# Kernel optimization log

Hardware: AMD Instinct MI355X
Metric: run time of the kernel (lower is better)

The kernel has to match this reference:

```python
import jax, jax.numpy as jnp
import numpy as np

C, P, H, W, BS = 256, 2, 128, 128, 4
NH, DH = 16, 16
NPATCH = (H // P) * (W // P)   # 4096
NTOK = NPATCH + 1              # 4097 with cls token
NMASK = int((1 - 0.75) * NTOK) # 1024 kept (visible) tokens
PRED = 512
NUM_BLOCKS = 1

def _sincos_pos_embed(embed_dim, h, w):
    # faithful port of get_2d_sincos_pos_embed
    def emb1d(d, pos):
        omega = np.arange(d // 2, dtype=np.float64) / (d / 2.0)
        omega = 1.0 / 10000 ** omega
        out = np.einsum('m,d->md', pos.reshape(-1), omega)
        return np.concatenate([np.sin(out), np.cos(out)], axis=1)
    gh = np.arange(h, dtype=np.float32)
    gw = np.arange(w, dtype=np.float32)
    grid = np.stack(np.meshgrid(gw, gh), axis=0).reshape(2, 1, h, w)
    emb = np.concatenate([emb1d(embed_dim // 2, grid[0]), emb1d(embed_dim // 2, grid[1])], axis=1)
    return jnp.asarray(emb, jnp.float32)  # [h*w, embed_dim]

def _ln(x, g, b, eps=1e-5):
    mu = x.mean(-1, keepdims=True)
    var = ((x - mu) ** 2).mean(-1, keepdims=True)
    return (x - mu) * jax.lax.rsqrt(var + eps) * g + b

def _gelu(x):
    return jax.nn.gelu(x, approximate=False)  # torch nn.GELU default (erf)

def _attn(x, qkv_w, qkv_b, proj_w, proj_b, nq_g, nq_b, nk_g, nk_b):
    bs, n, c = x.shape
    qkv = x @ qkv_w + qkv_b
    q, k, v = jnp.split(qkv, 3, axis=-1)
    heads = lambda t: t.reshape(bs, n, NH, DH).transpose(0, 2, 1, 3)  # [b,h,n,d]
    q, k, v = heads(q), heads(k), heads(v)
    q = _ln(q, nq_g, nq_b)  # per-head-dim QK LayerNorm
    k = _ln(k, nk_g, nk_b)
    score = jnp.einsum('bhnd,bhmd->bhnm', q, k) / np.float32(np.sqrt(DH))
    attn = jax.nn.softmax(score, axis=-1)
    attn_map = attn.mean(axis=1)[:, 0, 1:]  # [b, n-1]
    out = jnp.einsum('bhnm,bhmd->bhnd', attn, v)
    out = out.transpose(0, 2, 1, 3).reshape(bs, n, c)
    return out @ proj_w + proj_b, attn_map

def _forward(mask_index, x, Wp, bp, cls, qkv_w, qkv_b, proj_w, proj_b, nq_g, nq_b, nk_g, nk_b,
             conv_w, conv_b, ca1_w, ca1_b, ca2_w, ca2_b, mlp1_w, mlp1_b, mlp2_w, mlp2_b,
             node_w, ln0_g, ln0_b, h1_w, h1_b, ln1_g, ln1_b, h2_w, h2_b, ln2_g, ln2_b,
             h3_w, h3_b, pr_w, pr_b):
    bs = x.shape[0]
    # PatchEmbed: conv stride=kernel=P expressed as reshape + einsum
    xp = x.reshape(bs, 3, H // P, P, W // P, P)
    tok = jnp.einsum('bchpwq,ocpq->bohw', xp, Wp) + bp[None, :, None, None]
    tok = tok.reshape(bs, C, NPATCH).transpose(0, 2, 1)  # [b, l, c]
    tok = tok + _sincos_pos_embed(C, H // P, W // P)[None]
    tok = jnp.concatenate([jnp.broadcast_to(cls, (bs, 1, C)), tok], axis=1)  # prepend cls
    # mask_img: keep NMASK tokens per the precomputed permutation prefix
    m = jnp.take_along_axis(tok, mask_index[:, :, None], axis=1)  # [b, NMASK, C]

    attn_map = None
    for blk in range(NUM_BLOCKS):
        feat = m[..., None]  # feature_list: [b, l, c, width]
        for i in range(4):
            j = blk * 4 + i
            xl = feat[..., -1]
            o1 = _gelu(xl @ conv_w[j] + conv_b[j])  # Conv1x1Act
            gate = jax.nn.sigmoid(jax.nn.relu(xl @ ca1_w[j] + ca1_b[j]) @ ca2_w[j] + ca2_b[j])
            o2 = gate * xl                           # ChannelAttention
            o4 = _gelu(xl @ mlp1_w[j] + mlp1_b[j]) @ mlp2_w[j] + mlp2_b[j]  # MLP
            cat = jnp.concatenate([feat, jnp.stack([o1, o2, xl, o4], axis=-1)], axis=-1)  # width 5+i
            wmix = jax.nn.softmax(node_w[j, :5 + i] / 0.01)
            mixed = jnp.einsum('blcn,n->blc', cat, wmix)
            a_out, attn_map = _attn(mixed, qkv_w[j], qkv_b[j], proj_w[j], proj_b[j],
                                    nq_g[j], nq_b[j], nk_g[j], nk_b[j])
            xo = a_out + mixed  # residual
            feat = jnp.concatenate([feat, xo[..., None]], axis=-1)
        m = xo
    # Predict_head (tokenwise)
    h = _ln(m, ln0_g, ln0_b)
    h = h @ h1_w + h1_b
    h = _ln(h, ln1_g, ln1_b)
    h = h @ h2_w + h2_b
    h = _ln(h, ln2_g, ln2_b)
    h = h @ h3_w + h3_b
    return h @ pr_w + pr_b  # [b, NMASK, PRED]

def setup_inputs():
    key = jax.random.key(0)
    ks = iter(jax.random.split(key, 64))
    rn = lambda shape, s=0.02: jax.random.normal(next(ks), shape, jnp.float32) * s
    noise = jax.random.normal(next(ks), (BS, NTOK))
    mask_index = jnp.argsort(noise, axis=-1)[:, :NMASK].astype(jnp.int32)
    return dict(
        x=jax.random.normal(next(ks), (BS, 3, H, W), jnp.float32),
        mask_index=mask_index,
        Wp=rn((C, 3, P, P)), bp=jnp.zeros((C,)), cls=rn((1, 1, C)),
        qkv_w=rn((4, C, 3 * C)), qkv_b=jnp.zeros((4, 3 * C)),
        proj_w=rn((4, C, C)), proj_b=jnp.zeros((4, C)),
        nq_g=jnp.ones((4, DH)), nq_b=jnp.zeros((4, DH)),
        nk_g=jnp.ones((4, DH)), nk_b=jnp.zeros((4, DH)),
        conv_w=rn((4, C, C)), conv_b=jnp.zeros((4, C)),
        ca1_w=rn((4, C, C // 16)), ca1_b=jnp.zeros((4, C // 16)),
        ca2_w=rn((4, C // 16, C)), ca2_b=jnp.zeros((4, C)),
        mlp1_w=rn((4, C, 4 * C)), mlp1_b=jnp.zeros((4, 4 * C)),
        mlp2_w=rn((4, 4 * C, C)), mlp2_b=jnp.zeros((4, C)),
        node_w=jax.random.normal(next(ks), (4, 8), jnp.float32),
        ln0_g=jnp.ones((C,)), ln0_b=jnp.zeros((C,)),
        h1_w=rn((C, 2048)), h1_b=jnp.zeros((2048,)),
        ln1_g=jnp.ones((2048,)), ln1_b=jnp.zeros((2048,)),
        h2_w=rn((2048, 256)), h2_b=jnp.zeros((256,)),
        ln2_g=jnp.ones((256,)), ln2_b=jnp.zeros((256,)),
        h3_w=rn((256, 2048)), h3_b=jnp.zeros((2048,)),
        pr_w=rn((2048, PRED)), pr_b=jnp.zeros((PRED,)),
    )

def reference(x, mask_index, Wp, bp, cls, qkv_w, qkv_b, proj_w, proj_b, nq_g, nq_b, nk_g, nk_b,
              conv_w, conv_b, ca1_w, ca1_b, ca2_w, ca2_b, mlp1_w, mlp1_b, mlp2_w, mlp2_b,
              node_w, ln0_g, ln0_b, h1_w, h1_b, ln1_g, ln1_b, h2_w, h2_b, ln2_g, ln2_b,
              h3_w, h3_b, pr_w, pr_b):
    return _forward(mask_index, x, Wp, bp, cls, qkv_w, qkv_b, proj_w, proj_b, nq_g, nq_b, nk_g, nk_b,
                    conv_w, conv_b, ca1_w, ca1_b, ca2_w, ca2_b, mlp1_w, mlp1_b, mlp2_w, mlp2_b,
                    node_w, ln0_g, ln0_b, h1_w, h1_b, ln1_g, ln1_b, h2_w, h2_b, ln2_g, ln2_b,
                    h3_w, h3_b, pr_w, pr_b)
```

## Files before the change

kernel.cpp:

```cpp
#include <hip/hip_runtime.h>
#include <math.h>
#include <cstddef>

#define RTOK 4096
#define CDIM 256
#define NHEAD 16
#define DHEAD 16
#define SEQ 1024
#define BSZ 4

#define ACT_NONE 0
#define ACT_GELU 1

typedef short short8 __attribute__((ext_vector_type(8)));
typedef float f32x4  __attribute__((ext_vector_type(4)));
typedef _Float16 half8 __attribute__((ext_vector_type(8)));
typedef _Float16 half4 __attribute__((ext_vector_type(4)));

__device__ __forceinline__ float gelu_erf(float x) {
    return 0.5f * x * (1.0f + erff(x * 0.70710678118654752f));
}
__device__ __forceinline__ unsigned short f2b(float f) {
    unsigned u = __float_as_uint(f);
    unsigned r = (u + 0x7FFFu + ((u >> 16) & 1u)) >> 16;
    return (unsigned short)r;
}
__device__ __forceinline__ float b2f(unsigned short u) {
    return __uint_as_float((unsigned)u << 16);
}
__device__ __forceinline__ void gld16(const unsigned short* g, unsigned short* l) {
    __builtin_amdgcn_global_load_lds(
        (const __attribute__((address_space(1))) unsigned int*)g,
        (__attribute__((address_space(3))) unsigned int*)l, 16, 0, 0);
}
__device__ __forceinline__ float node_wsel(const float* nwp, int cnt, int widx) {
    float ww[8];
    float mx = -1e30f;
    for (int t = 0; t < cnt; ++t) { ww[t] = nwp[t] * 100.0f; mx = fmaxf(mx, ww[t]); }
    float ssum = 0.0f;
    for (int t = 0; t < cnt; ++t) { ww[t] = expf(ww[t] - mx); ssum += ww[t]; }
    return ww[widx] / ssum;
}

struct WtSeg { const float* in; unsigned short* out; int K, N, ntx, tpz, zin, zout; };
struct WtTab { WtSeg s[9]; int cum[10]; };

__global__ __launch_bounds__(256) void wtrans_all(WtTab tab)
{
    int g = blockIdx.x;
    int si = 0;
    #pragma unroll
    for (int i = 0; i < 8; ++i) if (g >= tab.cum[i + 1]) si = i + 1;
    WtSeg sg = tab.s[si];
    int t = g - tab.cum[si];
    int z = t / sg.tpz, r = t % sg.tpz;
    int kb = (r % sg.ntx) * 32, nb = (r / sg.ntx) * 32;
    const float* in = sg.in + (size_t)z * sg.zin;
    unsigned short* out = sg.out + (size_t)z * sg.zout;

    __shared__ float tt[32][33];
    int tx = threadIdx.x & 31, ty = threadIdx.x >> 5;
    #pragma unroll
    for (int rr = 0; rr < 4; ++rr) {
        int kk = ty * 4 + rr;
        tt[kk][tx] = in[(size_t)(kb + kk) * sg.N + nb + tx];
    }
    __syncthreads();
    #pragma unroll
    for (int rr = 0; rr < 4; ++rr) {
        int nn = ty * 4 + rr;
        out[(size_t)(nb + nn) * sg.K + kb + tx] = f2b(tt[tx][nn]);
    }
}

__global__ __launch_bounds__(256) void embed_kernel(
    const float* __restrict__ x, const int* __restrict__ mask_index,
    const float* __restrict__ Wp, const float* __restrict__ bp,
    const float* __restrict__ cls,
    float* __restrict__ out, unsigned short* __restrict__ outb)
{
    int row = blockIdx.x;
    int b = row >> 10;
    int c = threadIdx.x;
    int idx = mask_index[row];
    if (idx == 0) {
        float v = cls[c];
        out[(size_t)row * 256 + c] = v;
        outb[(size_t)row * 256 + c] = f2b(v);
        return;
    }
    int p  = idx - 1;
    int ph = p >> 6, pw = p & 63;

    __shared__ float xs[12];
    if (c < 12) {
        int ch = c >> 2, r = (c >> 1) & 1, q = c & 1;
        xs[c] = x[(((size_t)b * 3 + ch) * 128 + (ph * 2 + r)) * 128 + (pw * 2 + q)];
    }
    __syncthreads();

    float acc = bp[c];
    #pragma unroll
    for (int t = 0; t < 12; ++t) acc += xs[t] * Wp[c * 12 + t];

    int part = c >> 6, cc = c & 63;
    double omega = exp((double)cc * -0.14391156831212787);
    double posv  = (part < 2) ? (double)pw : (double)ph;
    double a     = posv * omega;
    double e     = ((part & 1) == 0) ? sin(a) : cos(a);
    float v = acc + (float)e;
    out[(size_t)row * 256 + c] = v;
    outb[(size_t)row * 256 + c] = f2b(v);
}

template<int MT, int ACT, bool RES, bool FOUT, int BMODE, bool SPLIT, int NW>
__global__ __launch_bounds__(256) void gemm_mfma(
    const unsigned short* __restrict__ A, const unsigned short* __restrict__ Bt,
    const float* __restrict__ bias, const float* __restrict__ bias1,
    const float* __restrict__ Rsd,
    float* __restrict__ C, unsigned short* __restrict__ Cb,
    int M, int N, int K, int N0,
    const float* __restrict__ nwp, int ncnt, int widx)
{
    constexpr int BM = 64 * MT;
    __shared__ __align__(16) unsigned short As[BM * 64];
    __shared__ __align__(16) unsigned short Bs[64 * 64];
    int tid = threadIdx.x;
    int w = tid >> 6, lane = tid & 63;
    int l15 = lane & 15, q = lane >> 4;

    int gx = gridDim.x, gy = gridDim.y;
    int L = blockIdx.x + gx * blockIdx.y;
    int xcd = L & 7, j = L >> 3;
    int by = xcd * (gy >> 3) + j / gx;
    int bx = j - (j / gx) * gx;
    int row0 = by * BM, col0 = bx * 64;

    f32x4 acc[MT][4];
    #pragma unroll
    for (int mt = 0; mt < MT; ++mt)
        #pragma unroll
        for (int nt = 0; nt < 4; ++nt)
            acc[mt][nt] = (f32x4){0.f, 0.f, 0.f, 0.f};

    for (int kb = 0; kb < K; kb += 64) {
        __syncthreads();
        #pragma unroll
        for (int t = 0; t < 2 * MT; ++t) {
            int slot = tid + t * 256;
            int r = slot >> 3;
            int s = (slot & 7) ^ (r & 7);
            gld16(A + (size_t)(row0 + r) * K + kb + s * 8, &As[slot * 8]);
        }
        #pragma unroll
        for (int t = 0; t < 2; ++t) {
            int slot = tid + t * 256;
            int r = slot >> 3;
            int s = (slot & 7) ^ (r & 7);
            gld16(Bt + (size_t)(col0 + r) * K + kb + s * 8, &Bs[slot * 8]);
        }
        __syncthreads();

        #pragma unroll
        for (int hh = 0; hh < 2; ++hh) {
            short8 af[MT];
            #pragma unroll
            for (int mt = 0; mt < MT; ++mt) {
                int R = w * 16 * MT + mt * 16 + l15;
                int c = hh * 4 + q;
                af[mt] = *(const short8*)&As[R * 64 + ((c ^ (R & 7)) << 3)];
            }
            #pragma unroll
            for (int nt = 0; nt < 4; ++nt) {
                int R = nt * 16 + l15;
                int c = hh * 4 + q;
                short8 bf = *(const short8*)&Bs[R * 64 + ((c ^ (R & 7)) << 3)];
                #pragma unroll
                for (int mt = 0; mt < MT; ++mt)
                    acc[mt][nt] = __builtin_amdgcn_mfma_f32_16x16x32_bf16(
                        af[mt], bf, acc[mt][nt], 0, 0, 0);
            }
        }
    }

    float wsel = 0.0f;
    if (NW > 0) wsel = node_wsel(nwp, ncnt, widx);

    #pragma unroll
    for (int mt = 0; mt < MT; ++mt) {
        #pragma unroll
        for (int nt = 0; nt < 4; ++nt) {
            #pragma unroll
            for (int reg = 0; reg < 4; ++reg) {
                int row = row0 + w * 16 * MT + mt * 16 + q * 4 + reg;
                int col = col0 + nt * 16 + l15;
                if (SPLIT) {
                    float v = acc[mt][nt][reg] +
                              (col < N0 ? bias[col] : bias1[col - N0]);
                    if (ACT == ACT_GELU) v = gelu_erf(v);
                    if (col < N0) {
                        if (NW == 1) C[(size_t)row * N0 + col] += wsel * v;
                        else         C[(size_t)row * N0 + col] = v;
                    } else {
                        Cb[(size_t)row * (N - N0) + (col - N0)] = f2b(v);
                    }
                } else {
                    float v = acc[mt][nt][reg] + bias[col];
                    if (ACT == ACT_GELU) v = gelu_erf(v);
                    if (NW == 2) v = wsel * v + Rsd[(size_t)row * N + col];
                    else if (RES) v += Rsd[(size_t)row * N + col];
                    if (FOUT) C[(size_t)row * N + col] = v;
                    if (BMODE == 1) Cb[(size_t)row * N + col] = f2b(v);
                    if (BMODE == 2) {
                        _Float16 hv = (_Float16)v;
                        Cb[(size_t)row * N + col] = *(unsigned short*)&hv;
                    }
                }
            }
        }
    }
}

__global__ __launch_bounds__(256) void chanattn_kernel(
    const float* __restrict__ xl,
    const float* f0, const float* f1, const float* f2,
    const float* __restrict__ ca1w, const float* __restrict__ ca1b,
    const float* __restrict__ ca2w, const float* __restrict__ ca2b,
    const float* __restrict__ node_w, int cnt,
    float* __restrict__ MIX)
{
    __shared__ float xs[256];
    __shared__ float sm16[16];
    size_t row = blockIdx.x;
    int tid = threadIdx.x;
    xs[tid] = xl[row * 256 + tid];
    __syncthreads();

    int h = tid >> 4, part = tid & 15;
    float p = 0.f;
    #pragma unroll
    for (int i = 0; i < 16; ++i)
        p += xs[part * 16 + i] * ca1w[(part * 16 + i) * 16 + h];
    p += __shfl_down(p, 8, 16);
    p += __shfl_down(p, 4, 16);
    p += __shfl_down(p, 2, 16);
    p += __shfl_down(p, 1, 16);
    if (part == 0) sm16[h] = fmaxf(p + ca1b[h], 0.0f);
    __syncthreads();

    float g = ca2b[tid];
    #pragma unroll
    for (int hh = 0; hh < 16; ++hh) g += sm16[hh] * ca2w[hh * 256 + tid];
    g = 1.0f / (1.0f + expf(-g));
    float o2 = g * xs[tid];

    float ww[8];
    float mx = -1e30f;
    for (int t = 0; t < cnt; ++t) { ww[t] = node_w[t] * 100.0f; mx = fmaxf(mx, ww[t]); }
    float ssum = 0.0f;
    for (int t = 0; t < cnt; ++t) { ww[t] = expf(ww[t] - mx); ssum += ww[t]; }
    float inv = 1.0f / ssum;
    int j = cnt - 5;
    float acc = (ww[j] + ww[j + 3]) * inv * xs[tid] + ww[j + 2] * inv * o2;
    const float* fs[3] = {f0, f1, f2};
    for (int t = 0; t < j; ++t) acc += ww[t] * inv * fs[t][row * 256 + tid];
    MIX[row * 256 + tid] = acc;
}

__global__ __launch_bounds__(256) void ln256_kernel(
    const float* __restrict__ in, unsigned short* __restrict__ outb,
    const float* __restrict__ g, const float* __restrict__ bb)
{
    int row = blockIdx.x * 4 + (threadIdx.x >> 6);
    int lane = threadIdx.x & 63;
    f32x4 xv = *(const f32x4*)(in + (size_t)row * 256 + lane * 4);
    float s = xv[0] + xv[1] + xv[2] + xv[3];
    #pragma unroll
    for (int off = 1; off < 64; off <<= 1) s += __shfl_xor(s, off, 64);
    float mu = s * (1.0f / 256.0f);
    float d0 = xv[0]-mu, d1 = xv[1]-mu, d2 = xv[2]-mu, d3 = xv[3]-mu;
    float s2 = d0*d0 + d1*d1 + d2*d2 + d3*d3;
    #pragma unroll
    for (int off = 1; off < 64; off <<= 1) s2 += __shfl_xor(s2, off, 64);
    float rstd = rsqrtf(s2 * (1.0f / 256.0f) + 1e-5f);
    f32x4 gv = *(const f32x4*)(g + lane * 4);
    f32x4 bv = *(const f32x4*)(bb + lane * 4);
    ushort4 o;
    o.x = f2b(d0 * rstd * gv[0] + bv[0]);
    o.y = f2b(d1 * rstd * gv[1] + bv[1]);
    o.z = f2b(d2 * rstd * gv[2] + bv[2]);
    o.w = f2b(d3 * rstd * gv[3] + bv[3]);
    *(ushort4*)(outb + (size_t)row * 256 + lane * 4) = o;
}

__global__ __launch_bounds__(256) void lnwb_kernel(
    const unsigned short* __restrict__ in, unsigned short* __restrict__ outb,
    const float* __restrict__ g, const float* __restrict__ bb, int N)
{
    __shared__ float sm[4];
    size_t row = blockIdx.x;
    const unsigned short* xr = in + row * N;
    int lane = threadIdx.x & 63, wid = threadIdx.x >> 6;

    float s = 0.0f;
    for (int i = threadIdx.x; i < N; i += 256) s += b2f(xr[i]);
    #pragma unroll
    for (int off = 32; off > 0; off >>= 1) s += __shfl_down(s, off, 64);
    if (lane == 0) sm[wid] = s;
    __syncthreads();
    float mu = (sm[0] + sm[1] + sm[2] + sm[3]) / N;
    __syncthreads();

    float s2 = 0.0f;
    for (int i = threadIdx.x; i < N; i += 256) { float d = b2f(xr[i]) - mu; s2 += d * d; }
    #pragma unroll
    for (int off = 32; off > 0; off >>= 1) s2 += __shfl_down(s2, off, 64);
    if (lane == 0) sm[wid] = s2;
    __syncthreads();
    float var = (sm[0] + sm[1] + sm[2] + sm[3]) / N;
    float rstd = rsqrtf(var + 1e-5f);

    for (int i = threadIdx.x; i < N; i += 256)
        outb[row * N + i] = f2b((b2f(xr[i]) - mu) * rstd * g[i] + bb[i]);
}

__global__ __launch_bounds__(256) void attn_prep(
    const unsigned short* __restrict__ qkvh,
    const float* __restrict__ nqg, const float* __restrict__ nqb,
    const float* __restrict__ nkg, const float* __restrict__ nkb,
    unsigned short* __restrict__ Qph, unsigned short* __restrict__ Kph,
    unsigned short* __restrict__ Vph)
{
    int b = blockIdx.x >> 6;
    int tokbase = (blockIdx.x & 63) * 16;
    int tid = threadIdx.x;
    int tl = tid >> 4, h = tid & 15;
    int tok = tokbase + tl;
    const _Float16* qkv = (const _Float16*)qkvh;
    const _Float16* rowp = qkv + ((size_t)(b * 1024 + tok)) * 768;
    _Float16* Qp = (_Float16*)Qph;
    _Float16* Kp = (_Float16*)Kph;
    _Float16* Vp = (_Float16*)Vph;
    const float QSC = 0.25f * 1.44269504088896340736f;

    __shared__ _Float16 vt[16][16][17];

    {
        half8 a0 = *(const half8*)(rowp + h * 16);
        half8 a1 = *(const half8*)(rowp + h * 16 + 8);
        float v[16];
        #pragma unroll
        for (int e = 0; e < 8; ++e) { v[e] = (float)a0[e]; v[8 + e] = (float)a1[e]; }
        float mu = 0.f;
        #pragma unroll
        for (int d = 0; d < 16; ++d) mu += v[d];
        mu *= (1.0f / 16.0f);
        float var = 0.f;
        #pragma unroll
        for (int d = 0; d < 16; ++d) { float t = v[d] - mu; var += t * t; }
        var *= (1.0f / 16.0f);
        float rstd = rsqrtf(var + 1e-5f);
        half8 o0, o1;
        #pragma unroll
        for (int e = 0; e < 8; ++e) {
            o0[e] = (_Float16)(((v[e] - mu) * rstd * nqg[e] + nqb[e]) * QSC);
            o1[e] = (_Float16)(((v[8+e] - mu) * rstd * nqg[8+e] + nqb[8+e]) * QSC);
        }
        _Float16* qo = Qp + ((size_t)(b * 16 + h) * 1024 + tok) * 16;
        *(half8*)qo = o0;
        *(half8*)(qo + 8) = o1;
    }
    {
        half8 a0 = *(const half8*)(rowp + 256 + h * 16);
        half8 a1 = *(const half8*)(rowp + 256 + h * 16 + 8);
        float v[16];
        #pragma unroll
        for (int e = 0; e < 8; ++e) { v[e] = (float)a0[e]; v[8 + e] = (float)a1[e]; }
        float mu = 0.f;
        #pragma unroll
        for (int d = 0; d < 16; ++d) mu += v[d];
        mu *= (1.0f / 16.0f);
        float var = 0.f;
        #pragma unroll
        for (int d = 0; d < 16; ++d) { float t = v[d] - mu; var += t * t; }
        var *= (1.0f / 16.0f);
        float rstd = rsqrtf(var + 1e-5f);
        half8 o0, o1;
        #pragma unroll
        for (int e = 0; e < 8; ++e) {
            o0[e] = (_Float16)((v[e] - mu) * rstd * nkg[e] + nkb[e]);
            o1[e] = (_Float16)((v[8+e] - mu) * rstd * nkg[8+e] + nkb[8+e]);
        }
        _Float16* ko = Kp + ((size_t)(b * 16 + h) * 1024 + tok) * 16;
        *(half8*)ko = o0;
        *(half8*)(ko + 8) = o1;
    }
    {
        half8 a0 = *(const half8*)(rowp + 512 + h * 16);
        half8 a1 = *(const half8*)(rowp + 512 + h * 16 + 8);
        #pragma unroll
        for (int e = 0; e < 8; ++e) { vt[tl][h][e] = a0[e]; vt[tl][h][8 + e] = a1[e]; }
    }
    __syncthreads();
    {
        int h2 = tid >> 4, d = tid & 15;
        half8 o0, o1;
        #pragma unroll
        for (int t = 0; t < 8; ++t) { o0[t] = vt[t][h2][d]; o1[t] = vt[8 + t][h2][d]; }
        _Float16* vo = Vp + ((size_t)(b * 16 + h2) * 16 + d) * 1024 + tokbase;
        *(half8*)vo = o0;
        *(half8*)(vo + 8) = o1;
    }
}

__global__ __launch_bounds__(256) void attn_kernel(
    const unsigned short* __restrict__ Qph, const unsigned short* __restrict__ Kph,
    const unsigned short* __restrict__ Vph,
    unsigned short* __restrict__ outb)
{
    int qt = blockIdx.x, h = blockIdx.y, b = blockIdx.z;
    int bh = b * 16 + h;
    int tid = threadIdx.x;
    int w = tid >> 6, lane = tid & 63;
    int l15 = lane & 15, quad = lane >> 4;
    const _Float16* Qp = (const _Float16*)Qph + (size_t)bh * 1024 * 16;
    const _Float16* Kp = (const _Float16*)Kph + (size_t)bh * 1024 * 16;
    const _Float16* Vp = (const _Float16*)Vph + (size_t)bh * 16 * 1024;

    __shared__ __align__(16) _Float16 Qs[64 * 40];
    __shared__ __align__(16) _Float16 Kb[128 * 40];
    __shared__ __align__(16) _Float16 Vt[16 * 136];
    __shared__ __align__(16) _Float16 Ps[4][16 * 136];

    uint4 z4 = {0, 0, 0, 0};
    if (tid < 64) {
        *(uint4*)&Qs[tid * 40 + 16] = z4;
        *(uint4*)&Qs[tid * 40 + 24] = z4;
    } else if (tid < 192) {
        int r = tid - 64;
        *(uint4*)&Kb[r * 40 + 16] = z4;
        *(uint4*)&Kb[r * 40 + 24] = z4;
    }
    if (tid < 128) {
        int r = tid >> 1, part = tid & 1;
        *(uint4*)&Qs[r * 40 + part * 8] =
            *(const uint4*)(Qp + (size_t)(qt * 64 + r) * 16 + part * 8);
    }
    __syncthreads();

    half8 bq = *(const half8*)&Qs[(w * 16 + l15) * 40 + quad * 8];
    float mst = -1e30f, lst = 0.f;
    f32x4 acco = (f32x4){0.f, 0.f, 0.f, 0.f};

    for (int kt = 0; kt < 8; ++kt) {
        __syncthreads();
        {
            int r = tid >> 1, part = tid & 1;
            *(uint4*)&Kb[r * 40 + part * 8] =
                *(const uint4*)(Kp + (size_t)(kt * 128 + r) * 16 + part * 8);
        }
        {
            int d = tid >> 4, kk8 = tid & 15;
            *(uint4*)&Vt[d * 136 + kk8 * 8] =
                *(const uint4*)(Vp + (size_t)d * 1024 + kt * 128 + kk8 * 8);
        }
        __syncthreads();

        f32x4 sacc[8];
        #pragma unroll
        for (int ni = 0; ni < 8; ++ni) {
            half8 ak = *(const half8*)&Kb[(ni * 16 + l15) * 40 + quad * 8];
            sacc[ni] = __builtin_amdgcn_mfma_f32_16x16x32_f16(
                ak, bq, (f32x4){0.f, 0.f, 0.f, 0.f}, 0, 0, 0);
        }
        half8 bv[4];
        #pragma unroll
        for (int c = 0; c < 4; ++c)
            bv[c] = *(const half8*)&Vt[l15 * 136 + c * 32 + quad * 8];

        float rm = sacc[0][0];
        #pragma unroll
        for (int ni = 0; ni < 8; ++ni)
            #pragma unroll
            for (int reg = 0; reg < 4; ++reg)
                rm = fmaxf(rm, sacc[ni][reg]);
        rm = fmaxf(rm, __shfl_xor(rm, 16, 64));
        rm = fmaxf(rm, __shfl_xor(rm, 32, 64));
        float mn  = fmaxf(mst, rm);
        float cor = exp2f(mst - mn);
        mst = mn;
        lst *= cor;
        #pragma unroll
        for (int reg = 0; reg < 4; ++reg) {
            float cR = __shfl(cor, (lane & 48) + quad * 4 + reg, 64);
            acco[reg] *= cR;
        }
        float lsum = 0.f;
        #pragma unroll
        for (int ni = 0; ni < 8; ++ni) {
            half4 ph;
            #pragma unroll
            for (int reg = 0; reg < 4; ++reg) {
                float p = exp2f(sacc[ni][reg] - mn);
                lsum += p;
                ph[reg] = (_Float16)p;
            }
            *(half4*)&Ps[w][l15 * 136 + ni * 16 + quad * 4] = ph;
        }
        lsum += __shfl_xor(lsum, 16, 64);
        lsum += __shfl_xor(lsum, 32, 64);
        lst += lsum;

        #pragma unroll
        for (int c = 0; c < 4; ++c) {
            half8 p0 = *(const half8*)&Ps[w][l15 * 136 + c * 32 + quad * 8];
            acco = __builtin_amdgcn_mfma_f32_16x16x32_f16(p0, bv[c], acco, 0, 0, 0);
        }
    }

    #pragma unroll
    for (int reg = 0; reg < 4; ++reg) {
        float lR = __shfl(lst, (lane & 48) + quad * 4 + reg, 64);
        float o = acco[reg] / lR;
        int row = b * 1024 + qt * 64 + w * 16 + quad * 4 + reg;
        outb[(size_t)row * 256 + h * 16 + l15] = f2b(o);
    }
}

extern "C" void kernel_launch(void* const* d_in, const int* in_sizes, int n_in,
                              void* d_out, int out_size, void* d_ws, size_t ws_size,
                              hipStream_t stream)
{
    const float* x          = (const float*)d_in[0];
    const int*   mask_index = (const int*)  d_in[1];
    const float* Wp         = (const float*)d_in[2];
    const float* bp         = (const float*)d_in[3];
    const float* cls        = (const float*)d_in[4];
    const float* qkv_w      = (const float*)d_in[5];
    const float* qkv_b      = (const float*)d_in[6];
    const float* proj_w     = (const float*)d_in[7];
    const float* proj_b     = (const float*)d_in[8];
    const float* nq_g       = (const float*)d_in[9];
    const float* nq_b       = (const float*)d_in[10];
    const float* nk_g       = (const float*)d_in[11];
    const float* nk_b       = (const float*)d_in[12];
    const float* conv_w     = (const float*)d_in[13];
    const float* conv_b     = (const float*)d_in[14];
    const float* ca1_w      = (const float*)d_in[15];
    const float* ca1_b      = (const float*)d_in[16];
    const float* ca2_w      = (const float*)d_in[17];
    const float* ca2_b      = (const float*)d_in[18];
    const float* mlp1_w     = (const float*)d_in[19];
    const float* mlp1_b     = (const float*)d_in[20];
    const float* mlp2_w     = (const float*)d_in[21];
    const float* mlp2_b     = (const float*)d_in[22];
    const float* node_w     = (const float*)d_in[23];
    const float* ln0_g      = (const float*)d_in[24];
    const float* ln0_b      = (const float*)d_in[25];
    const float* h1_w       = (const float*)d_in[26];
    const float* h1_b       = (const float*)d_in[27];
    const float* ln1_g      = (const float*)d_in[28];
    const float* ln1_b      = (const float*)d_in[29];
    const float* h2_w       = (const float*)d_in[30];
    const float* h2_b       = (const float*)d_in[31];
    const float* ln2_g      = (const float*)d_in[32];
    const float* ln2_b      = (const float*)d_in[33];
    const float* h3_w       = (const float*)d_in[34];
    const float* h3_b       = (const float*)d_in[35];
    const float* pr_w       = (const float*)d_in[36];
    const float* pr_b       = (const float*)d_in[37];
    float* out = (float*)d_out;

    char* base = (char*)d_ws;
    size_t off = 0;
    auto alloc = [&](size_t bytes) -> char* {
        char* p = base + off;
        off += (bytes + 255) & ~(size_t)255;
        return p;
    };
    const size_t RC = (size_t)RTOK * CDIM;
    float* F[5];
    unsigned short* Fb[5];
    for (int i = 0; i < 5; ++i) F[i] = (float*)alloc(RC * 4);
    for (int i = 0; i < 5; ++i) Fb[i] = (unsigned short*)alloc(RC * 2);
    float* MIX = (float*)alloc(RC * 4);
    unsigned short* MIXb = (unsigned short*)alloc(RC * 2);
    unsigned short* AOb  = (unsigned short*)alloc(RC * 2);
    unsigned short* BIGH = (unsigned short*)alloc((size_t)RTOK * 768 * 2);
    unsigned short* Qp   = (unsigned short*)alloc((size_t)RTOK * 256 * 2);
    unsigned short* Kp   = (unsigned short*)alloc((size_t)RTOK * 256 * 2);
    unsigned short* Vp   = (unsigned short*)alloc((size_t)RTOK * 256 * 2);
    unsigned short* H1b  = (unsigned short*)alloc((size_t)RTOK * 2048 * 2);
    unsigned short* MIDU = (unsigned short*)alloc((size_t)RTOK * 2048 * 2);
    unsigned short* L0b  = (unsigned short*)alloc(RC * 2);
    unsigned short* L2b  = (unsigned short*)alloc(RC * 2);
    unsigned short* H3b  = (unsigned short*)alloc((size_t)RTOK * 2048 * 2);
    unsigned short* cm1b  = (unsigned short*)alloc((size_t)4 * 1280 * 256 * 2);
    unsigned short* qkvb  = (unsigned short*)alloc((size_t)4 * 768 * 256 * 2);
    unsigned short* projb = (unsigned short*)alloc((size_t)4 * 256 * 256 * 2);
    unsigned short* mlp2b = (unsigned short*)alloc((size_t)4 * 256 * 1024 * 2);
    unsigned short* h1b   = (unsigned short*)alloc((size_t)2048 * 256 * 2);
    unsigned short* h2b   = (unsigned short*)alloc((size_t)256 * 2048 * 2);
    unsigned short* h3b   = (unsigned short*)alloc((size_t)2048 * 256 * 2);
    unsigned short* prb   = (unsigned short*)alloc((size_t)512 * 2048 * 2);

    {
        WtTab tab;
        int c = 0, idx = 0;
        auto seg = [&](const float* in, unsigned short* outp, int K, int N,
                       int z, int zin, int zout) {
            WtSeg s; s.in = in; s.out = outp; s.K = K; s.N = N;
            s.ntx = K / 32; s.tpz = (K / 32) * (N / 32);
            s.zin = zin; s.zout = zout;
            tab.s[idx] = s; tab.cum[idx] = c;
            c += s.tpz * z; ++idx;
        };
        seg(conv_w, cm1b,         256, 256,  4, 256 * 256,  1280 * 256);
        seg(mlp1_w, cm1b + 65536, 256, 1024, 4, 256 * 1024, 1280 * 256);
        seg(qkv_w,  qkvb,  256, 768,  4, 256 * 768,  768 * 256);
        seg(proj_w, projb, 256, 256,  4, 256 * 256,  256 * 256);
        seg(mlp2_w, mlp2b, 1024, 256, 4, 1024 * 256, 256 * 1024);
        seg(h1_w, h1b, 256, 2048, 1, 0, 0);
        seg(h2_w, h2b, 2048, 256, 1, 0, 0);
        seg(h3_w, h3b, 256, 2048, 1, 0, 0);
        seg(pr_w, prb, 2048, 512, 1, 0, 0);
        tab.cum[9] = c;
        wtrans_all<<<c, 256, 0, stream>>>(tab);
    }

    embed_kernel<<<RTOK, 256, 0, stream>>>(x, mask_index, Wp, bp, cls, F[0], Fb[0]);

    for (int j = 0; j < 4; ++j) {
        const float* xl = F[j];
        const unsigned short* xlb = Fb[j];
        chanattn_kernel<<<RTOK, 256, 0, stream>>>(
            xl, F[0], F[1], F[2],
            ca1_w + (size_t)j * 256 * 16, ca1_b + j * 16,
            ca2_w + (size_t)j * 16 * 256, ca2_b + j * 256,
            node_w + j * 8, 5 + j, MIX);
        gemm_mfma<2, ACT_GELU, false, false, 0, true, 1><<<dim3(20, 32), 256, 0, stream>>>(
            xlb, cm1b + (size_t)j * 1280 * 256, conv_b + j * 256, mlp1_b + j * 1024,
            nullptr, MIX, MIDU, RTOK, 1280, 256, 256, node_w + j * 8, 5 + j, j + 1);
        gemm_mfma<1, ACT_NONE, false, true, 1, false, 2><<<dim3(4, 64), 256, 0, stream>>>(
            MIDU, mlp2b + (size_t)j * 256 * 1024, mlp2_b + j * 256, nullptr, MIX,
            MIX, MIXb, RTOK, 256, 1024, 0, node_w + j * 8, 5 + j, j + 4);
        gemm_mfma<2, ACT_NONE, false, false, 2, false, 0><<<dim3(12, 32), 256, 0, stream>>>(
            MIXb, qkvb + (size_t)j * 768 * 256, qkv_b + j * 768, nullptr, nullptr,
            nullptr, BIGH, RTOK, 768, 256, 0, nullptr, 0, 0);
        attn_prep<<<256, 256, 0, stream>>>(
            BIGH, nq_g + j * 16, nq_b + j * 16, nk_g + j * 16, nk_b + j * 16,
            Qp, Kp, Vp);
        attn_kernel<<<dim3(16, NHEAD, BSZ), 256, 0, stream>>>(Qp, Kp, Vp, AOb);
        gemm_mfma<1, ACT_NONE, true, true, 1, false, 0><<<dim3(4, 64), 256, 0, stream>>>(
            AOb, projb + (size_t)j * 256 * 256, proj_b + j * 256, nullptr, MIX,
            F[j + 1], Fb[j + 1], RTOK, 256, 256, 0, nullptr, 0, 0);
    }

    ln256_kernel<<<1024, 256, 0, stream>>>(F[4], L0b, ln0_g, ln0_b);
    gemm_mfma<2, ACT_NONE, false, false, 1, false, 0><<<dim3(32, 32), 256, 0, stream>>>(
        L0b, h1b, h1_b, nullptr, nullptr, nullptr, H1b, RTOK, 2048, 256, 0,
        nullptr, 0, 0);
    lnwb_kernel<<<RTOK, 256, 0, stream>>>(H1b, MIDU, ln1_g, ln1_b, 2048);
    gemm_mfma<1, ACT_NONE, false, true, 0, false, 0><<<dim3(4, 64), 256, 0, stream>>>(
        MIDU, h2b, h2_b, nullptr, nullptr, MIX, nullptr, RTOK, 256, 2048, 0,
        nullptr, 0, 0);
    ln256_kernel<<<1024, 256, 0, stream>>>(MIX, L2b, ln2_g, ln2_b);
    gemm_mfma<2, ACT_NONE, false, false, 1, false, 0><<<dim3(32, 32), 256, 0, stream>>>(
        L2b, h3b, h3_b, nullptr, nullptr, nullptr, H3b, RTOK, 2048, 256, 0,
        nullptr, 0, 0);
    gemm_mfma<1, ACT_NONE, false, true, 0, false, 0><<<dim3(8, 64), 256, 0, stream>>>(
        H3b, prb, pr_b, nullptr, nullptr, out, nullptr, RTOK, 512, 2048, 0,
        nullptr, 0, 0);
}
```

Measured before the change: 717.0 us.

## Fuse QK LayerNorm and head scatter into QKV GEMM epilogue

Replaces the generic QKV GEMM plus separate attn_prep kernel with a dedicated GEMM whose epilogue computes per-head Q/K LayerNorm through 16-lane shuffles and writes Q, K, V directly in per-head token-major layout. This removes the intermediate 4096x768 fp16 buffer round-trip and one kernel launch per block. V is now stored token-major, so the attention kernel transposes V into shared memory while loading it. The cost is scattered 2-byte epilogue stores and an LDS transpose with possible bank conflicts in the attention inner loop.

```diff
diff --git a/kernel.cpp b/kernel.cpp
--- a/kernel.cpp
+++ b/kernel.cpp
@@ -221,6 +221,120 @@
     }
 }
 
+__global__ __launch_bounds__(256) void gemm_qkv(
+    const unsigned short* __restrict__ A, const unsigned short* __restrict__ Bt,
+    const float* __restrict__ bias,
+    const float* __restrict__ nqg, const float* __restrict__ nqb,
+    const float* __restrict__ nkg, const float* __restrict__ nkb,
+    unsigned short* __restrict__ Qp, unsigned short* __restrict__ Kp,
+    unsigned short* __restrict__ Vp, int M, int N, int K)
+{
+    __shared__ __align__(16) unsigned short As[128 * 64];
+    __shared__ __align__(16) unsigned short Bs[64 * 64];
+    int tid = threadIdx.x;
+    int w = tid >> 6, lane = tid & 63;
+    int l15 = lane & 15, q = lane >> 4;
+
+    int gx = gridDim.x, gy = gridDim.y;
+    int L = blockIdx.x + gx * blockIdx.y;
+    int xcd = L & 7, j = L >> 3;
+    int by = xcd * (gy >> 3) + j / gx;
+    int bx = j - (j / gx) * gx;
+    int row0 = by * 128, col0 = bx * 64;
+
+    f32x4 acc[2][4];
+    #pragma unroll
+    for (int mt = 0; mt < 2; ++mt)
+        #pragma unroll
+        for (int nt = 0; nt < 4; ++nt)
+            acc[mt][nt] = (f32x4){0.f, 0.f, 0.f, 0.f};
+
+    for (int kb = 0; kb < K; kb += 64) {
+        __syncthreads();
+        #pragma unroll
+        for (int t = 0; t < 4; ++t) {
+            int slot = tid + t * 256;
+            int r = slot >> 3;
+            int s = (slot & 7) ^ (r & 7);
+            gld16(A + (size_t)(row0 + r) * K + kb + s * 8, &As[slot * 8]);
+        }
+        #pragma unroll
+        for (int t = 0; t < 2; ++t) {
+            int slot = tid + t * 256;
+            int r = slot >> 3;
+            int s = (slot & 7) ^ (r & 7);
+            gld16(Bt + (size_t)(col0 + r) * K + kb + s * 8, &Bs[slot * 8]);
+        }
+        __syncthreads();
+
+        #pragma unroll
+        for (int hh = 0; hh < 2; ++hh) {
+            short8 af[2];
+            #pragma unroll
+            for (int mt = 0; mt < 2; ++mt) {
+                int R = w * 32 + mt * 16 + l15;
+                int c = hh * 4 + q;
+                af[mt] = *(const short8*)&As[R * 64 + ((c ^ (R & 7)) << 3)];
+            }
+            #pragma unroll
+            for (int nt = 0; nt < 4; ++nt) {
+                int R = nt * 16 + l15;
+                int c = hh * 4 + q;
+                short8 bf = *(const short8*)&Bs[R * 64 + ((c ^ (R & 7)) << 3)];
+                #pragma unroll
+                for (int mt = 0; mt < 2; ++mt)
+                    acc[mt][nt] = __builtin_amdgcn_mfma_f32_16x16x32_bf16(
+                        af[mt], bf, acc[mt][nt], 0, 0, 0);
+            }
+        }
+    }
+
+    const float QSC = 0.25f * 1.44269504088896340736f;
+    float qg = nqg[l15], qb2 = nqb[l15];
+    float kg = nkg[l15], kb2 = nkb[l15];
+
+    #pragma unroll
+    for (int mt = 0; mt < 2; ++mt) {
+        #pragma unroll
+        for (int nt = 0; nt < 4; ++nt) {
+            int colg = col0 + nt * 16;
+            int region = colg >> 8;
+            int h = (colg >> 4) & 15;
+            #pragma unroll
+            for (int reg = 0; reg < 4; ++reg) {
+                int row = row0 + w * 32 + mt * 16 + q * 4 + reg;
+                float v = acc[mt][nt][reg] + bias[colg + l15];
+                _Float16 hv;
+                if (region == 2) {
+                    hv = (_Float16)v;
+                } else {
+                    float s = v;
+                    s += __shfl_xor(s, 1, 16);
+                    s += __shfl_xor(s, 2, 16);
+                    s += __shfl_xor(s, 4, 16);
+                    s += __shfl_xor(s, 8, 16);
+                    float mu = s * (1.0f / 16.0f);
+                    float dd = v - mu;
+                    float s2 = dd * dd;
+                    s2 += __shfl_xor(s2, 1, 16);
+                    s2 += __shfl_xor(s2, 2, 16);
+                    s2 += __shfl_xor(s2, 4, 16);
+                    s2 += __shfl_xor(s2, 8, 16);
+                    float rstd = rsqrtf(s2 * (1.0f / 16.0f) + 1e-5f);
+                    float o = (region == 0)
+                        ? (dd * rstd * qg + qb2) * QSC
+                        : (dd * rstd * kg + kb2);
+                    hv = (_Float16)o;
+                }
+                int b = row >> 10, tok = row & 1023;
+                unsigned short* dst = (region == 0) ? Qp : (region == 1 ? Kp : Vp);
+                dst[(((size_t)(b * 16 + h)) * 1024 + tok) * 16 + l15] =
+                    *(unsigned short*)&hv;
+            }
+        }
+    }
+}
+
 __global__ __launch_bounds__(256) void chanattn_kernel(
     const float* __restrict__ xl,
     const float* f0, const float* f1, const float* f2,
@@ -324,95 +438,6 @@
         outb[row * N + i] = f2b((b2f(xr[i]) - mu) * rstd * g[i] + bb[i]);
 }
 
-__global__ __launch_bounds__(256) void attn_prep(
-    const unsigned short* __restrict__ qkvh,
-    const float* __restrict__ nqg, const float* __restrict__ nqb,
-    const float* __restrict__ nkg, const float* __restrict__ nkb,
-    unsigned short* __restrict__ Qph, unsigned short* __restrict__ Kph,
-    unsigned short* __restrict__ Vph)
-{
-    int b = blockIdx.x >> 6;
-    int tokbase = (blockIdx.x & 63) * 16;
-    int tid = threadIdx.x;
-    int tl = tid >> 4, h = tid & 15;
-    int tok = tokbase + tl;
-    const _Float16* qkv = (const _Float16*)qkvh;
-    const _Float16* rowp = qkv + ((size_t)(b * 1024 + tok)) * 768;
-    _Float16* Qp = (_Float16*)Qph;
-    _Float16* Kp = (_Float16*)Kph;
-    _Float16* Vp = (_Float16*)Vph;
-    const float QSC = 0.25f * 1.44269504088896340736f;
-
-    __shared__ _Float16 vt[16][16][17];
-
-    {
-        half8 a0 = *(const half8*)(rowp + h * 16);
-        half8 a1 = *(const half8*)(rowp + h * 16 + 8);
-        float v[16];
-        #pragma unroll
-        for (int e = 0; e < 8; ++e) { v[e] = (float)a0[e]; v[8 + e] = (float)a1[e]; }
-        float mu = 0.f;
-        #pragma unroll
-        for (int d = 0; d < 16; ++d) mu += v[d];
-        mu *= (1.0f / 16.0f);
-        float var = 0.f;
-        #pragma unroll
-        for (int d = 0; d < 16; ++d) { float t = v[d] - mu; var += t * t; }
-        var *= (1.0f / 16.0f);
-        float rstd = rsqrtf(var + 1e-5f);
-        half8 o0, o1;
-        #pragma unroll
-        for (int e = 0; e < 8; ++e) {
-            o0[e] = (_Float16)(((v[e] - mu) * rstd * nqg[e] + nqb[e]) * QSC);
-            o1[e] = (_Float16)(((v[8+e] - mu) * rstd * nqg[8+e] + nqb[8+e]) * QSC);
-        }
-        _Float16* qo = Qp + ((size_t)(b * 16 + h) * 1024 + tok) * 16;
-        *(half8*)qo = o0;
-        *(half8*)(qo + 8) = o1;
-    }
-    {
-        half8 a0 = *(const half8*)(rowp + 256 + h * 16);
-        half8 a1 = *(const half8*)(rowp + 256 + h * 16 + 8);
-        float v[16];
-        #pragma unroll
-        for (int e = 0; e < 8; ++e) { v[e] = (float)a0[e]; v[8 + e] = (float)a1[e]; }
-        float mu = 0.f;
-        #pragma unroll
-        for (int d = 0; d < 16; ++d) mu += v[d];
-        mu *= (1.0f / 16.0f);
-        float var = 0.f;
-        #pragma unroll
-        for (int d = 0; d < 16; ++d) { float t = v[d] - mu; var += t * t; }
-        var *= (1.0f / 16.0f);
-        float rstd = rsqrtf(var + 1e-5f);
-        half8 o0, o1;
-        #pragma unroll
-        for (int e = 0; e < 8; ++e) {
-            o0[e] = (_Float16)((v[e] - mu) * rstd * nkg[e] + nkb[e]);
-            o1[e] = (_Float16)((v[8+e] - mu) * rstd * nkg[8+e] + nkb[8+e]);
-        }
-        _Float16* ko = Kp + ((size_t)(b * 16 + h) * 1024 + tok) * 16;
-        *(half8*)ko = o0;
-        *(half8*)(ko + 8) = o1;
-    }
-    {
-        half8 a0 = *(const half8*)(rowp + 512 + h * 16);
-        half8 a1 = *(const half8*)(rowp + 512 + h * 16 + 8);
-        #pragma unroll
-        for (int e = 0; e < 8; ++e) { vt[tl][h][e] = a0[e]; vt[tl][h][8 + e] = a1[e]; }
-    }
-    __syncthreads();
-    {
-        int h2 = tid >> 4, d = tid & 15;
-        half8 o0, o1;
-        #pragma unroll
-        for (int t = 0; t < 8; ++t) { o0[t] = vt[t][h2][d]; o1[t] = vt[8 + t][h2][d]; }
-        _Float16* vo = Vp + ((size_t)(b * 16 + h2) * 16 + d) * 1024 + tokbase;
-        *(half8*)vo = o0;
-        *(half8*)(vo + 8) = o1;
-    }
-}
-
 __global__ __launch_bounds__(256) void attn_kernel(
     const unsigned short* __restrict__ Qph, const unsigned short* __restrict__ Kph,
     const unsigned short* __restrict__ Vph,
@@ -425,7 +450,7 @@
     int l15 = lane & 15, quad = lane >> 4;
     const _Float16* Qp = (const _Float16*)Qph + (size_t)bh * 1024 * 16;
     const _Float16* Kp = (const _Float16*)Kph + (size_t)bh * 1024 * 16;
-    const _Float16* Vp = (const _Float16*)Vph + (size_t)bh * 16 * 1024;
+    const _Float16* Vp = (const _Float16*)Vph + (size_t)bh * 1024 * 16;
 
     __shared__ __align__(16) _Float16 Qs[64 * 40];
     __shared__ __align__(16) _Float16 Kb[128 * 40];
@@ -454,15 +479,21 @@
 
     for (int kt = 0; kt < 8; ++kt) {
         __syncthreads();
-        {
-            int r = tid >> 1, part = tid & 1;
-            *(uint4*)&Kb[r * 40 + part * 8] =
-                *(const uint4*)(Kp + (size_t)(kt * 128 + r) * 16 + part * 8);
-        }
-        {
-            int d = tid >> 4, kk8 = tid & 15;
-            *(uint4*)&Vt[d * 136 + kk8 * 8] =
-                *(const uint4*)(Vp + (size_t)d * 1024 + kt * 128 + kk8 * 8);
+        if (tid < 128) {
+            int r = tid;
+            const uint4* src = (const uint4*)(Kp + (size_t)(kt * 128 + r) * 16);
+            *(uint4*)&Kb[r * 40 + 0] = src[0];
+            *(uint4*)&Kb[r * 40 + 8] = src[1];
+        } else {
+            int r = tid - 128;
+            const _Float16* vp = Vp + (size_t)(kt * 128 + r) * 16;
+            half8 a0 = *(const half8*)(vp);
+            half8 a1 = *(const half8*)(vp + 8);
+            #pragma unroll
+            for (int e = 0; e < 8; ++e) {
+                Vt[e * 136 + r] = a0[e];
+                Vt[(8 + e) * 136 + r] = a1[e];
+            }
         }
         __syncthreads();
 
@@ -586,10 +617,9 @@
     float* MIX = (float*)alloc(RC * 4);
     unsigned short* MIXb = (unsigned short*)alloc(RC * 2);
     unsigned short* AOb  = (unsigned short*)alloc(RC * 2);
-    unsigned short* BIGH = (unsigned short*)alloc((size_t)RTOK * 768 * 2);
-    unsigned short* Qp   = (unsigned short*)alloc((size_t)RTOK * 256 * 2);
-    unsigned short* Kp   = (unsigned short*)alloc((size_t)RTOK * 256 * 2);
-    unsigned short* Vp   = (unsigned short*)alloc((size_t)RTOK * 256 * 2);
+    unsigned short* Qp   = (unsigned short*)alloc(RC * 2);
+    unsigned short* Kp   = (unsigned short*)alloc(RC * 2);
+    unsigned short* Vp   = (unsigned short*)alloc(RC * 2);
     unsigned short* H1b  = (unsigned short*)alloc((size_t)RTOK * 2048 * 2);
     unsigned short* MIDU = (unsigned short*)alloc((size_t)RTOK * 2048 * 2);
     unsigned short* L0b  = (unsigned short*)alloc(RC * 2);
@@ -644,12 +674,10 @@
         gemm_mfma<1, ACT_NONE, false, true, 1, false, 2><<<dim3(4, 64), 256, 0, stream>>>(
             MIDU, mlp2b + (size_t)j * 256 * 1024, mlp2_b + j * 256, nullptr, MIX,
             MIX, MIXb, RTOK, 256, 1024, 0, node_w + j * 8, 5 + j, j + 4);
-        gemm_mfma<2, ACT_NONE, false, false, 2, false, 0><<<dim3(12, 32), 256, 0, stream>>>(
-            MIXb, qkvb + (size_t)j * 768 * 256, qkv_b + j * 768, nullptr, nullptr,
-            nullptr, BIGH, RTOK, 768, 256, 0, nullptr, 0, 0);
-        attn_prep<<<256, 256, 0, stream>>>(
-            BIGH, nq_g + j * 16, nq_b + j * 16, nk_g + j * 16, nk_b + j * 16,
-            Qp, Kp, Vp);
+        gemm_qkv<<<dim3(12, 32), 256, 0, stream>>>(
+            MIXb, qkvb + (size_t)j * 768 * 256, qkv_b + j * 768,
+            nq_g + j * 16, nq_b + j * 16, nk_g + j * 16, nk_b + j * 16,
+            Qp, Kp, Vp, RTOK, 768, 256);
         attn_kernel<<<dim3(16, NHEAD, BSZ), 256, 0, stream>>>(Qp, Kp, Vp, AOb);
         gemm_mfma<1, ACT_NONE, true, true, 1, false, 0><<<dim3(4, 64), 256, 0, stream>>>(
             AOb, projb + (size_t)j * 256 * 256, proj_b + j * 256, nullptr, MIX,
```

Result: slower. 749.1 us (+4.5%).

## Double-buffer LDS tiles in MFMA GEMM to overlap loads with compute

Applied to the files above, without the earlier changes.

The GEMM main loop now uses two LDS buffers for the A and B tiles. It issues the global loads for the next 64-wide K chunk before computing on the current one, so memory latency can hide behind MFMA work. This doubles LDS use per block, which may lower occupancy. It assumes K is a multiple of 128. The workspace allocation change for Qp/Kp/Vp is cosmetic, since RC already equals RTOK*256.

```diff
diff --git a/kernel.cpp b/kernel.cpp
--- a/kernel.cpp
+++ b/kernel.cpp
@@ -123,8 +123,10 @@
     const float* __restrict__ nwp, int ncnt, int widx)
 {
     constexpr int BM = 64 * MT;
-    __shared__ __align__(16) unsigned short As[BM * 64];
-    __shared__ __align__(16) unsigned short Bs[64 * 64];
+    __shared__ __align__(16) unsigned short As0[BM * 64];
+    __shared__ __align__(16) unsigned short As1[BM * 64];
+    __shared__ __align__(16) unsigned short Bs0[64 * 64];
+    __shared__ __align__(16) unsigned short Bs1[64 * 64];
     int tid = threadIdx.x;
     int w = tid >> 6, lane = tid & 63;
     int l15 = lane & 15, q = lane >> 4;
@@ -143,45 +145,59 @@
         for (int nt = 0; nt < 4; ++nt)
             acc[mt][nt] = (f32x4){0.f, 0.f, 0.f, 0.f};
 
-    for (int kb = 0; kb < K; kb += 64) {
+#define G_ISSUE(AS, BS, KB)                                                   \
+    do {                                                                      \
+        _Pragma("unroll")                                                     \
+        for (int t = 0; t < 2 * MT; ++t) {                                    \
+            int slot = tid + t * 256;                                         \
+            int r = slot >> 3;                                                \
+            int s = (slot & 7) ^ (r & 7);                                     \
+            gld16(A + (size_t)(row0 + r) * K + (KB) + s * 8, &AS[slot * 8]);  \
+        }                                                                     \
+        _Pragma("unroll")                                                     \
+        for (int t = 0; t < 2; ++t) {                                         \
+            int slot = tid + t * 256;                                         \
+            int r = slot >> 3;                                                \
+            int s = (slot & 7) ^ (r & 7);                                     \
+            gld16(Bt + (size_t)(col0 + r) * K + (KB) + s * 8, &BS[slot * 8]); \
+        }                                                                     \
+    } while (0)
+
+#define G_COMPUTE(AS, BS)                                                     \
+    do {                                                                      \
+        _Pragma("unroll")                                                     \
+        for (int hh = 0; hh < 2; ++hh) {                                      \
+            short8 af[MT];                                                    \
+            _Pragma("unroll")                                                 \
+            for (int mt = 0; mt < MT; ++mt) {                                 \
+                int R = w * 16 * MT + mt * 16 + l15;                          \
+                int c = hh * 4 + q;                                           \
+                af[mt] = *(const short8*)&AS[R * 64 + ((c ^ (R & 7)) << 3)];  \
+            }                                                                 \
+            _Pragma("unroll")                                                 \
+            for (int nt = 0; nt < 4; ++nt) {                                  \
+                int R = nt * 16 + l15;                                        \
+                int c = hh * 4 + q;                                           \
+                short8 bf = *(const short8*)&BS[R * 64 + ((c ^ (R & 7)) << 3)];\
+                _Pragma("unroll")                                             \
+                for (int mt = 0; mt < MT; ++mt)                               \
+                    acc[mt][nt] = __builtin_amdgcn_mfma_f32_16x16x32_bf16(    \
+                        af[mt], bf, acc[mt][nt], 0, 0, 0);                    \
+            }                                                                 \
+        }                                                                     \
+    } while (0)
+
+    G_ISSUE(As0, Bs0, 0);
+    for (int kb = 0; kb < K; kb += 128) {
         __syncthreads();
-        #pragma unroll
-        for (int t = 0; t < 2 * MT; ++t) {
-            int slot = tid + t * 256;
-            int r = slot >> 3;
-            int s = (slot & 7) ^ (r & 7);
-            gld16(A + (size_t)(row0 + r) * K + kb + s * 8, &As[slot * 8]);
-        }
-        #pragma unroll
-        for (int t = 0; t < 2; ++t) {
-            int slot = tid + t * 256;
-            int r = slot >> 3;
-            int s = (slot & 7) ^ (r & 7);
-            gld16(Bt + (size_t)(col0 + r) * K + kb + s * 8, &Bs[slot * 8]);
-        }
+        G_ISSUE(As1, Bs1, kb + 64);
+        G_COMPUTE(As0, Bs0);
         __syncthreads();
-
-        #pragma unroll
-        for (int hh = 0; hh < 2; ++hh) {
-            short8 af[MT];
-            #pragma unroll
-            for (int mt = 0; mt < MT; ++mt) {
-                int R = w * 16 * MT + mt * 16 + l15;
-                int c = hh * 4 + q;
-                af[mt] = *(const short8*)&As[R * 64 + ((c ^ (R & 7)) << 3)];
-            }
-            #pragma unroll
-            for (int nt = 0; nt < 4; ++nt) {
-                int R = nt * 16 + l15;
-                int c = hh * 4 + q;
-                short8 bf = *(const short8*)&Bs[R * 64 + ((c ^ (R & 7)) << 3)];
-                #pragma unroll
-                for (int mt = 0; mt < MT; ++mt)
-                    acc[mt][nt] = __builtin_amdgcn_mfma_f32_16x16x32_bf16(
-                        af[mt], bf, acc[mt][nt], 0, 0, 0);
-            }
-        }
-    }
+        if (kb + 128 < K) G_ISSUE(As0, Bs0, kb + 128);
+        G_COMPUTE(As1, Bs1);
+    }
+#undef G_ISSUE
+#undef G_COMPUTE
 
     float wsel = 0.0f;
     if (NW > 0) wsel = node_wsel(nwp, ncnt, widx);
@@ -587,9 +603,9 @@
     unsigned short* MIXb = (unsigned short*)alloc(RC * 2);
     unsigned short* AOb  = (unsigned short*)alloc(RC * 2);
     unsigned short* BIGH = (unsigned short*)alloc((size_t)RTOK * 768 * 2);
-    unsigned short* Qp   = (unsigned short*)alloc((size_t)RTOK * 256 * 2);
-    unsigned short* Kp   = (unsigned short*)alloc((size_t)RTOK * 256 * 2);
-    unsigned short* Vp   = (unsigned short*)alloc((size_t)RTOK * 256 * 2);
+    unsigned short* Qp   = (unsigned short*)alloc(RC * 2);
+    unsigned short* Kp   = (unsigned short*)alloc(RC * 2);
+    unsigned short* Vp   = (unsigned short*)alloc(RC * 2);
     unsigned short* H1b  = (unsigned short*)alloc((size_t)RTOK * 2048 * 2);
     unsigned short* MIDU = (unsigned short*)alloc((size_t)RTOK * 2048 * 2);
     unsigned short* L0b  = (unsigned short*)alloc(RC * 2);
```

Measured after the change: 671.6 us. 1.07x faster.
